# Kernel optimization log

Hardware: AMD Instinct MI355X
Metric: run time of the kernel (lower is better)

Reference implementation:

```python
import jax, jax.numpy as jnp
import numpy as np

B, L, INP, HID, NCLS = 512, 256, 300, 256, 5  # trees, leaves/tree, embed dim, hidden, classes


def setup_inputs() -> dict:
    key = jax.random.key(0)
    ks = jax.random.split(key, 7)
    s_in = 1.0 / np.sqrt(INP).astype(np.float32)
    s_h = 1.0 / np.sqrt(HID).astype(np.float32)
    # W_leaf order: [inp_gate, out_gate, upd_gate]
    # W_nl order:  [inp_ln, inp_rn, fo_l_l, fo_l_r, fo_r_l, fo_r_r, out_ln, out_rn, upd_ln, upd_rn]
    return {
        "embeddings": jax.random.normal(ks[0], (B, L, INP), jnp.float32),
        "W_leaf": jax.random.uniform(ks[1], (3, INP, HID), jnp.float32, -s_in, s_in),
        "b_leaf": jax.random.uniform(ks[2], (3, HID), jnp.float32, -s_in, s_in),
        "W_nl": jax.random.uniform(ks[3], (10, HID, HID), jnp.float32, -s_h, s_h),
        "b_nl": jax.random.uniform(ks[4], (10, HID), jnp.float32, -s_h, s_h),
        "W_out": jax.random.uniform(ks[5], (HID, NCLS), jnp.float32, -s_h, s_h),
        "b_out": jax.random.uniform(ks[6], (NCLS,), jnp.float32, -s_h, s_h),
    }


def reference(embeddings, W_leaf, b_leaf, W_nl, b_nl, W_out, b_out):
    sig, tanh = jax.nn.sigmoid, jnp.tanh
    # ---- leaf nodes (depth 0), batched over all B*L leaves ----
    pre = jnp.einsum('bli,gih->blgh', embeddings, W_leaf) + b_leaf  # [B,L,3,H]
    i_g = sig(pre[:, :, 0])
    o_g = sig(pre[:, :, 1])
    u_g = tanh(pre[:, :, 2])
    c = i_g * u_g                      # [B,L,H]
    h = o_g * sig(c)                   # note: leaf uses sigmoid(cell), as in torch code
    logits = [jnp.einsum('bnh,hc->bnc', h, W_out) + b_out]
    # ---- internal nodes, level-synchronous ----
    Wl = W_nl[0::2]                    # [5,H,H] acting on left hidden
    Wr = W_nl[1::2]                    # [5,H,H] acting on right hidden
    bb = b_nl[0::2] + b_nl[1::2]       # [5,H]
    n = L
    while n > 1:
        lc, rc = c[:, 0::2], c[:, 1::2]
        lh, rh = h[:, 0::2], h[:, 1::2]
        pre = (jnp.einsum('bnh,ghk->bngk', lh, Wl)
               + jnp.einsum('bnh,ghk->bngk', rh, Wr) + bb)  # [B,n/2,5,H]
        inp_g = sig(pre[:, :, 0])
        fol_g = sig(pre[:, :, 1])
        for_g = sig(pre[:, :, 2])
        out_g = sig(pre[:, :, 3])
        upd_g = tanh(pre[:, :, 4])
        c = inp_g * upd_g + fol_g * lc + for_g * rc
        h = out_g * tanh(c)
        logits.append(jnp.einsum('bnh,hc->bnc', h, W_out) + b_out)
        n //= 2
    # per-node class scores for all 2L-1 nodes (leaves first, root last)
    return jnp.concatenate(logits, axis=1)  # [B, 2L-1, NCLS]
```

## Files before the change

### kernel.cpp

```cpp
#include <hip/hip_runtime.h>
#include <hip/hip_bf16.h>


#define HID 256

typedef __attribute__((ext_vector_type(8))) short short8;
typedef __attribute__((ext_vector_type(4))) float f32x4;
typedef __attribute__((ext_vector_type(4))) unsigned short ushort4v;

__device__ __forceinline__ float rcpf(float x) { return __builtin_amdgcn_rcpf(x); }
__device__ __forceinline__ float sigf(float x) { return rcpf(1.0f + __expf(-x)); }
__device__ __forceinline__ float tanhf_(float x) { return 2.0f * rcpf(1.0f + __expf(-2.0f * x)) - 1.0f; }
__device__ __forceinline__ unsigned short f2bf(float f) {
    __hip_bfloat16 b = __float2bfloat16(f);
    return *(unsigned short*)&b;
}
__device__ __forceinline__ void gload_lds16(const void* g, void* l) {
    __builtin_amdgcn_global_load_lds(
        (const __attribute__((address_space(1))) unsigned int*)g,
        (__attribute__((address_space(3))) unsigned int*)l, 16, 0, 0);
}

template <int NG, int K, bool LEAF>
__global__ __launch_bounds__(256, 3) void gemm_gates(
    const unsigned short* __restrict__ A,
    const unsigned short* __restrict__ BT,
    const float* __restrict__ bias,
    const float* __restrict__ cprev,
    float* __restrict__ cout,
    unsigned short* __restrict__ hout,
    const float* __restrict__ W_out,
    float* __restrict__ out,
    int log2n, int off)
{
    constexpr int CS  = 32;
    constexpr int BN  = NG * CS;
    constexpr int NK  = K / 64;
    constexpr int NBW = BN / 32;
    constexpr int ABUF = 128 * 128;

    __shared__ char smem[2 * ABUF + BN * 128];
    char* Bs = smem + 2 * ABUF;

    const int t = threadIdx.x;
    const int lane = t & 63;
    const int w = t >> 6;
    const int wm = w >> 1, wn = w & 1;
    const int row0 = blockIdx.x * 128;
    const int cb = blockIdx.y;

    const int l3 = lane >> 3;
    const unsigned int swsrc = (unsigned int)(((lane & 7) ^ l3) * 16);
    unsigned int a_src[4];
    unsigned int b_src[NBW];
#pragma unroll
    for (int q = 0; q < 4; ++q)
        a_src[q] = (unsigned int)(row0 + (w * 4 + q) * 8 + l3) * (K * 2) + swsrc;
#pragma unroll
    for (int q = 0; q < NBW; ++q)
        b_src[q] = (unsigned int)(cb * BN + (w * NBW + q) * 8 + l3) * (K * 2) + swsrc;

    const int swz0 = ((lane >> 4) ^ (lane & 7)) * 16;
    const int swz1 = (((lane >> 4) + 4) ^ (lane & 7)) * 16;
    const int aoff = (wm * 64 + (lane & 15)) * 128;
    const int boff = (wn * 16 + (lane & 15)) * 128;

    f32x4 acc[4][NG] = {};

    auto STAGE_A = [&](int buf, int kt) {
        char* As = smem + buf * ABUF;
        const unsigned int k0b = (unsigned int)kt * 128;
#pragma unroll
        for (int q = 0; q < 4; ++q)
            gload_lds16((const char*)A + (size_t)(a_src[q] + k0b),
                        As + (w * 4 + q) * 1024);
    };
    auto STAGE_B = [&](int kt) {
        const unsigned int k0b = (unsigned int)kt * 128;
#pragma unroll
        for (int q = 0; q < NBW; ++q)
            gload_lds16((const char*)BT + (size_t)(b_src[q] + k0b),
                        Bs + (w * NBW + q) * 1024);
    };

    STAGE_A(0, 0);
    STAGE_B(0);
    asm volatile("s_waitcnt vmcnt(0)" ::: "memory");
    __builtin_amdgcn_s_barrier();
    asm volatile("" ::: "memory");

#pragma unroll
    for (int kt = 0; kt < NK; ++kt) {
        const int cur = kt & 1;
        if (kt + 1 < NK) STAGE_A(cur ^ 1, kt + 1);
        const char* As = smem + cur * ABUF;
#pragma unroll
        for (int ks = 0; ks < 2; ++ks) {
            const int sw = ks ? swz1 : swz0;
            short8 a[4];
#pragma unroll
            for (int mf = 0; mf < 4; ++mf)
                a[mf] = *(const short8*)(As + aoff + mf * 2048 + sw);
#pragma unroll
            for (int g = 0; g < NG; ++g) {
                short8 b = *(const short8*)(Bs + g * (CS * 128) + boff + sw);
#pragma unroll
                for (int mf = 0; mf < 4; ++mf)
                    acc[mf][g] = __builtin_amdgcn_mfma_f32_16x16x32_bf16(
                        a[mf], b, acc[mf][g], 0, 0, 0);
            }
        }
        asm volatile("" ::: "memory");
        __builtin_amdgcn_s_barrier();
        asm volatile("" ::: "memory");
        if (kt + 1 < NK) {
            STAGE_B(kt + 1);
            asm volatile("s_waitcnt vmcnt(0)" ::: "memory");
        }
        __builtin_amdgcn_s_barrier();
        asm volatile("" ::: "memory");
    }

    float* hs = (float*)smem;
    float* Ws = (float*)(smem + 128 * 33 * 4);
    for (int i = t; i < CS * 5; i += 256) Ws[i] = W_out[cb * CS * 5 + i];

#pragma unroll
    for (int mf = 0; mf < 4; ++mf) {
#pragma unroll
        for (int j = 0; j < 4; ++j) {
            const int rl = wm * 64 + mf * 16 + ((lane >> 4) << 2) + j;
            const int r = row0 + rl;
            const int cl = wn * 16 + (lane & 15);
            const int c = cb * CS + cl;
            float cv, hv;
            if constexpr (LEAF) {
                float p0 = acc[mf][0][j] + bias[c];
                float p1 = acc[mf][1][j] + bias[256 + c];
                float p2 = acc[mf][2][j] + bias[512 + c];
                cv = sigf(p0) * tanhf_(p2);
                hv = sigf(p1) * sigf(cv);
            } else {
                float p0 = acc[mf][0][j] + bias[c];
                float p1 = acc[mf][1][j] + bias[256 + c];
                float p2 = acc[mf][2][j] + bias[512 + c];
                float p3 = acc[mf][3][j] + bias[768 + c];
                float p4 = acc[mf][4][j] + bias[1024 + c];
                float lc = cprev[(size_t)r * 512 + c];
                float rc = cprev[(size_t)r * 512 + 256 + c];
                cv = sigf(p0) * tanhf_(p4) + sigf(p1) * lc + sigf(p2) * rc;
                hv = sigf(p3) * tanhf_(cv);
            }
            cout[(size_t)r * 256 + c] = cv;
            hout[(size_t)r * 256 + c] = f2bf(hv);
            hs[rl * 33 + cl] = hv;
        }
    }
    __syncthreads();

    const int nmask = (1 << log2n) - 1;
    for (int idx = t; idx < 128 * 5; idx += 256) {
        int rl = idx / 5, cls = idx - rl * 5;
        float s = 0.f;
#pragma unroll
        for (int c2 = 0; c2 < CS; ++c2)
            s = fmaf(hs[rl * 33 + c2], Ws[c2 * 5 + cls], s);
        int rg = row0 + rl;
        int b = rg >> log2n, jj = rg & nmask;
        atomicAdd(out + ((size_t)b * 511 + off + jj) * 5 + cls, s);
    }
}

__global__ __launch_bounds__(256) void prep_weights(
    const float* __restrict__ W_leaf, const float* __restrict__ W_nl,
    const float* __restrict__ b_nl, const float* __restrict__ b_out,
    unsigned short* __restrict__ BleafT, unsigned short* __restrict__ BlevT,
    float* __restrict__ bb, float* __restrict__ out)
{
    const int T1 = 768 * 320, T2 = 1280 * 512, T3 = 5 * 256, T4 = 261632 * 5;
    for (int idx = blockIdx.x * 256 + threadIdx.x; idx < T1 + T2 + T3 + T4;
         idx += gridDim.x * 256) {
        if (idx < T1) {
            int colp = idx / 320, k = idx % 320;
            int cbv = colp / 96, rem = colp % 96;
            int g = rem >> 5, cl = rem & 31;
            int c = cbv * 32 + cl;
            float v = (k < 300) ? W_leaf[((size_t)g * 300 + k) * 256 + c] : 0.0f;
            BleafT[(size_t)colp * 320 + k] = f2bf(v);
        } else if (idx < T1 + T2) {
            int i2 = idx - T1;
            int colp = i2 / 512, k = i2 % 512;
            int cb8 = colp / 160, rem = colp % 160;
            int g = rem >> 5, cl = rem & 31;
            int c = cb8 * 32 + cl;
            float v = W_nl[((size_t)(2 * g + (k >= 256)) * 256 + (k & 255)) * 256 + c];
            BlevT[(size_t)colp * 512 + k] = f2bf(v);
        } else if (idx < T1 + T2 + T3) {
            int i3 = idx - T1 - T2;
            bb[i3] = b_nl[(size_t)(i3 >> 8) * 512 + (i3 & 255)] +
                     b_nl[(size_t)(i3 >> 8) * 512 + 256 + (i3 & 255)];
        } else {
            int i4 = idx - T1 - T2 - T3;
            out[i4] = b_out[i4 % 5];
        }
    }
}

__global__ __launch_bounds__(256) void emb_to_bf16(
    const float* __restrict__ emb, unsigned short* __restrict__ embB)
{
    const int total = 131072 * 80;
    for (int idx = blockIdx.x * 256 + threadIdx.x; idx < total;
         idx += gridDim.x * 256) {
        int r = idx / 80, q = idx % 80;
        ushort4v o;
        if (q < 75) {
            const float4 v = *(const float4*)(emb + (size_t)r * 300 + q * 4);
            o.x = f2bf(v.x); o.y = f2bf(v.y); o.z = f2bf(v.z); o.w = f2bf(v.w);
        } else {
            o.x = 0; o.y = 0; o.z = 0; o.w = 0;
        }
        *(ushort4v*)(embB + (size_t)r * 320 + q * 4) = o;
    }
}

extern "C" void kernel_launch(void* const* d_in, const int* in_sizes, int n_in,
                              void* d_out, int out_size, void* d_ws, size_t ws_size,
                              hipStream_t stream) {
    const float* emb    = (const float*)d_in[0];
    const float* W_leaf = (const float*)d_in[1];
    const float* b_leaf = (const float*)d_in[2];
    const float* W_nl   = (const float*)d_in[3];
    const float* b_nl   = (const float*)d_in[4];
    const float* W_out  = (const float*)d_in[5];
    const float* b_out  = (const float*)d_in[6];
    float* out = (float*)d_out;

    char* ws = (char*)d_ws;
    unsigned short* embB   = (unsigned short*)(ws);
    unsigned short* BleafT = (unsigned short*)(ws + 83886080);
    unsigned short* BlevT  = (unsigned short*)(ws + 84377600);
    float*          bb     = (float*)(ws + 85688320);
    float*          cA     = (float*)(ws + 85693440);
    unsigned short* hA     = (unsigned short*)(ws + 219911168);
    float*          cB     = (float*)(ws + 287020032);
    unsigned short* hB     = (unsigned short*)(ws + 354128896);

    prep_weights<<<2048, 256, 0, stream>>>(W_leaf, W_nl, b_nl, b_out,
                                           BleafT, BlevT, bb, out);
    emb_to_bf16<<<2048, 256, 0, stream>>>(emb, embB);

    gemm_gates<3, 320, true><<<dim3(1024, 8), 256, 0, stream>>>(
        embB, BleafT, b_leaf, nullptr, cA, hA, W_out, out, 8, 0);

    const unsigned short* hp = hA;
    const float* cp = cA;
    int off = 256;
    for (int lev = 1; lev <= 8; ++lev) {
        int log2n = 8 - lev;
        int n = 1 << log2n;
        int M = 512 * n;
        float* cd = (lev & 1) ? cB : cA;
        unsigned short* hd = (lev & 1) ? hB : hA;
        gemm_gates<5, 512, false><<<dim3(M / 128, 8), 256, 0, stream>>>(
            hp, BlevT, bb, cp, cd, hd, W_out, out, log2n, off);
        cp = cd;
        hp = hd;
        off += n;
    }
}
```

Before: 512.5 us.

## Add large-tile 512-thread GEMM variant for leaf and early tree levels

Adds a gemm_big kernel using 256x(NG*64) tiles, 8 waves, a unified double-buffered A+B LDS stage and s_setprio around the MFMA bursts. It is used for the leaf level and for internal levels with M>=16384, with a matching column-permuted weight layout. Small levels keep the old 128-row kernel with the original weight layout. The aim is more reuse of each A/B tile and fewer redundant A loads across column blocks. In exchange it uses more LDS and registers per block (acc[8][5]), which cuts occupancy, and it stores two copies of the level weights.

```diff
diff --git a/kernel.cpp b/kernel.cpp
--- a/kernel.cpp
+++ b/kernel.cpp
@@ -22,7 +22,7 @@
 }
 
 template <int NG, int K, bool LEAF>
-__global__ __launch_bounds__(256, 3) void gemm_gates(
+__global__ __launch_bounds__(512, 2) void gemm_big(
     const unsigned short* __restrict__ A,
     const unsigned short* __restrict__ BT,
     const float* __restrict__ bias,
@@ -33,106 +33,96 @@
     float* __restrict__ out,
     int log2n, int off)
 {
-    constexpr int CS  = 32;
-    constexpr int BN  = NG * CS;
-    constexpr int NK  = K / 64;
-    constexpr int NBW = BN / 32;
-    constexpr int ABUF = 128 * 128;
-
-    __shared__ char smem[2 * ABUF + BN * 128];
-    char* Bs = smem + 2 * ABUF;
+    constexpr int BN   = NG * 64;
+    constexpr int NK   = K / 64;
+    constexpr int ABUF = 256 * 128;
+    constexpr int BBUF = BN * 128;
+    constexpr int BUF  = ABUF + BBUF;
+
+    __shared__ char smem[2 * BUF];
 
     const int t = threadIdx.x;
     const int lane = t & 63;
     const int w = t >> 6;
-    const int wm = w >> 1, wn = w & 1;
-    const int row0 = blockIdx.x * 128;
+    const int wm = w >> 2, wn = w & 3;
+    const int row0 = blockIdx.x * 256;
     const int cb = blockIdx.y;
 
     const int l3 = lane >> 3;
     const unsigned int swsrc = (unsigned int)(((lane & 7) ^ l3) * 16);
     unsigned int a_src[4];
-    unsigned int b_src[NBW];
+    unsigned int b_src[NG];
 #pragma unroll
     for (int q = 0; q < 4; ++q)
         a_src[q] = (unsigned int)(row0 + (w * 4 + q) * 8 + l3) * (K * 2) + swsrc;
 #pragma unroll
-    for (int q = 0; q < NBW; ++q)
-        b_src[q] = (unsigned int)(cb * BN + (w * NBW + q) * 8 + l3) * (K * 2) + swsrc;
+    for (int q = 0; q < NG; ++q)
+        b_src[q] = (unsigned int)(cb * BN + (w * NG + q) * 8 + l3) * (K * 2) + swsrc;
 
     const int swz0 = ((lane >> 4) ^ (lane & 7)) * 16;
     const int swz1 = (((lane >> 4) + 4) ^ (lane & 7)) * 16;
-    const int aoff = (wm * 64 + (lane & 15)) * 128;
-    const int boff = (wn * 16 + (lane & 15)) * 128;
-
-    f32x4 acc[4][NG] = {};
-
-    auto STAGE_A = [&](int buf, int kt) {
-        char* As = smem + buf * ABUF;
+    const int aoff = (wm * 128 + (lane & 15)) * 128;
+    const int boff = (wn * (NG * 16) + (lane & 15)) * 128;
+
+    f32x4 acc[8][NG] = {};
+
+    auto STAGE = [&](int buf, int kt) {
+        char* As = smem + buf * BUF;
+        char* Bs = As + ABUF;
         const unsigned int k0b = (unsigned int)kt * 128;
 #pragma unroll
         for (int q = 0; q < 4; ++q)
             gload_lds16((const char*)A + (size_t)(a_src[q] + k0b),
                         As + (w * 4 + q) * 1024);
+#pragma unroll
+        for (int q = 0; q < NG; ++q)
+            gload_lds16((const char*)BT + (size_t)(b_src[q] + k0b),
+                        Bs + (w * NG + q) * 1024);
     };
-    auto STAGE_B = [&](int kt) {
-        const unsigned int k0b = (unsigned int)kt * 128;
-#pragma unroll
-        for (int q = 0; q < NBW; ++q)
-            gload_lds16((const char*)BT + (size_t)(b_src[q] + k0b),
-                        Bs + (w * NBW + q) * 1024);
-    };
-
-    STAGE_A(0, 0);
-    STAGE_B(0);
-    asm volatile("s_waitcnt vmcnt(0)" ::: "memory");
-    __builtin_amdgcn_s_barrier();
-    asm volatile("" ::: "memory");
+
+    STAGE(0, 0);
+    __syncthreads();
 
 #pragma unroll
     for (int kt = 0; kt < NK; ++kt) {
         const int cur = kt & 1;
-        if (kt + 1 < NK) STAGE_A(cur ^ 1, kt + 1);
-        const char* As = smem + cur * ABUF;
+        const char* As = smem + cur * BUF;
+        const char* Bs = As + ABUF;
+        if (kt + 1 < NK) STAGE(cur ^ 1, kt + 1);
 #pragma unroll
         for (int ks = 0; ks < 2; ++ks) {
             const int sw = ks ? swz1 : swz0;
-            short8 a[4];
-#pragma unroll
-            for (int mf = 0; mf < 4; ++mf)
+            short8 a[8], b[NG];
+#pragma unroll
+            for (int mf = 0; mf < 8; ++mf)
                 a[mf] = *(const short8*)(As + aoff + mf * 2048 + sw);
 #pragma unroll
-            for (int g = 0; g < NG; ++g) {
-                short8 b = *(const short8*)(Bs + g * (CS * 128) + boff + sw);
-#pragma unroll
-                for (int mf = 0; mf < 4; ++mf)
+            for (int g = 0; g < NG; ++g)
+                b[g] = *(const short8*)(Bs + boff + g * 2048 + sw);
+            __builtin_amdgcn_s_setprio(1);
+#pragma unroll
+            for (int g = 0; g < NG; ++g)
+#pragma unroll
+                for (int mf = 0; mf < 8; ++mf)
                     acc[mf][g] = __builtin_amdgcn_mfma_f32_16x16x32_bf16(
-                        a[mf], b, acc[mf][g], 0, 0, 0);
-            }
-        }
-        asm volatile("" ::: "memory");
-        __builtin_amdgcn_s_barrier();
-        asm volatile("" ::: "memory");
-        if (kt + 1 < NK) {
-            STAGE_B(kt + 1);
-            asm volatile("s_waitcnt vmcnt(0)" ::: "memory");
-        }
-        __builtin_amdgcn_s_barrier();
-        asm volatile("" ::: "memory");
+                        a[mf], b[g], acc[mf][g], 0, 0, 0);
+            __builtin_amdgcn_s_setprio(0);
+        }
+        __syncthreads();
     }
 
     float* hs = (float*)smem;
-    float* Ws = (float*)(smem + 128 * 33 * 4);
-    for (int i = t; i < CS * 5; i += 256) Ws[i] = W_out[cb * CS * 5 + i];
-
-#pragma unroll
-    for (int mf = 0; mf < 4; ++mf) {
+    float* Ws = (float*)(smem + 256 * 65 * 4);
+    for (int i = t; i < 320; i += 512) Ws[i] = W_out[cb * 320 + i];
+
+    const int cl = wn * 16 + (lane & 15);
+    const int c = cb * 64 + cl;
+#pragma unroll
+    for (int mf = 0; mf < 8; ++mf) {
 #pragma unroll
         for (int j = 0; j < 4; ++j) {
-            const int rl = wm * 64 + mf * 16 + ((lane >> 4) << 2) + j;
+            const int rl = wm * 128 + mf * 16 + ((lane >> 4) << 2) + j;
             const int r = row0 + rl;
-            const int cl = wn * 16 + (lane & 15);
-            const int c = cb * CS + cl;
             float cv, hv;
             if constexpr (LEAF) {
                 float p0 = acc[mf][0][j] + bias[c];
@@ -153,6 +143,147 @@
             }
             cout[(size_t)r * 256 + c] = cv;
             hout[(size_t)r * 256 + c] = f2bf(hv);
+            hs[rl * 65 + cl] = hv;
+        }
+    }
+    __syncthreads();
+
+    const int nmask = (1 << log2n) - 1;
+    for (int idx = t; idx < 256 * 5; idx += 512) {
+        int rl = idx / 5, cls = idx - rl * 5;
+        float s = 0.f;
+#pragma unroll
+        for (int c2 = 0; c2 < 64; ++c2)
+            s = fmaf(hs[rl * 65 + c2], Ws[c2 * 5 + cls], s);
+        int rg = row0 + rl;
+        int b = rg >> log2n, jj = rg & nmask;
+        atomicAdd(out + ((size_t)b * 511 + off + jj) * 5 + cls, s);
+    }
+}
+
+template <int NG, int K>
+__global__ __launch_bounds__(256, 3) void gemm_small(
+    const unsigned short* __restrict__ A,
+    const unsigned short* __restrict__ BT,
+    const float* __restrict__ bias,
+    const float* __restrict__ cprev,
+    float* __restrict__ cout,
+    unsigned short* __restrict__ hout,
+    const float* __restrict__ W_out,
+    float* __restrict__ out,
+    int log2n, int off)
+{
+    constexpr int CS  = 32;
+    constexpr int BN  = NG * CS;
+    constexpr int NK  = K / 64;
+    constexpr int NBW = BN / 32;
+    constexpr int ABUF = 128 * 128;
+
+    __shared__ char smem[2 * ABUF + BN * 128];
+    char* Bs = smem + 2 * ABUF;
+
+    const int t = threadIdx.x;
+    const int lane = t & 63;
+    const int w = t >> 6;
+    const int wm = w >> 1, wn = w & 1;
+    const int row0 = blockIdx.x * 128;
+    const int cb = blockIdx.y;
+
+    const int l3 = lane >> 3;
+    const unsigned int swsrc = (unsigned int)(((lane & 7) ^ l3) * 16);
+    unsigned int a_src[4];
+    unsigned int b_src[NBW];
+#pragma unroll
+    for (int q = 0; q < 4; ++q)
+        a_src[q] = (unsigned int)(row0 + (w * 4 + q) * 8 + l3) * (K * 2) + swsrc;
+#pragma unroll
+    for (int q = 0; q < NBW; ++q)
+        b_src[q] = (unsigned int)(cb * BN + (w * NBW + q) * 8 + l3) * (K * 2) + swsrc;
+
+    const int swz0 = ((lane >> 4) ^ (lane & 7)) * 16;
+    const int swz1 = (((lane >> 4) + 4) ^ (lane & 7)) * 16;
+    const int aoff = (wm * 64 + (lane & 15)) * 128;
+    const int boff = (wn * 16 + (lane & 15)) * 128;
+
+    f32x4 acc[4][NG] = {};
+
+    auto STAGE_A = [&](int buf, int kt) {
+        char* As = smem + buf * ABUF;
+        const unsigned int k0b = (unsigned int)kt * 128;
+#pragma unroll
+        for (int q = 0; q < 4; ++q)
+            gload_lds16((const char*)A + (size_t)(a_src[q] + k0b),
+                        As + (w * 4 + q) * 1024);
+    };
+    auto STAGE_B = [&](int kt) {
+        const unsigned int k0b = (unsigned int)kt * 128;
+#pragma unroll
+        for (int q = 0; q < NBW; ++q)
+            gload_lds16((const char*)BT + (size_t)(b_src[q] + k0b),
+                        Bs + (w * NBW + q) * 1024);
+    };
+
+    STAGE_A(0, 0);
+    STAGE_B(0);
+    asm volatile("s_waitcnt vmcnt(0)" ::: "memory");
+    __builtin_amdgcn_s_barrier();
+    asm volatile("" ::: "memory");
+
+#pragma unroll
+    for (int kt = 0; kt < NK; ++kt) {
+        const int cur = kt & 1;
+        if (kt + 1 < NK) STAGE_A(cur ^ 1, kt + 1);
+        const char* As = smem + cur * ABUF;
+#pragma unroll
+        for (int ks = 0; ks < 2; ++ks) {
+            const int sw = ks ? swz1 : swz0;
+            short8 a[4];
+#pragma unroll
+            for (int mf = 0; mf < 4; ++mf)
+                a[mf] = *(const short8*)(As + aoff + mf * 2048 + sw);
+#pragma unroll
+            for (int g = 0; g < NG; ++g) {
+                short8 b = *(const short8*)(Bs + g * (CS * 128) + boff + sw);
+#pragma unroll
+                for (int mf = 0; mf < 4; ++mf)
+                    acc[mf][g] = __builtin_amdgcn_mfma_f32_16x16x32_bf16(
+                        a[mf], b, acc[mf][g], 0, 0, 0);
+            }
+        }
+        asm volatile("" ::: "memory");
+        __builtin_amdgcn_s_barrier();
+        asm volatile("" ::: "memory");
+        if (kt + 1 < NK) {
+            STAGE_B(kt + 1);
+            asm volatile("s_waitcnt vmcnt(0)" ::: "memory");
+        }
+        __builtin_amdgcn_s_barrier();
+        asm volatile("" ::: "memory");
+    }
+
+    float* hs = (float*)smem;
+    float* Ws = (float*)(smem + 128 * 33 * 4);
+    for (int i = t; i < CS * 5; i += 256) Ws[i] = W_out[cb * CS * 5 + i];
+
+#pragma unroll
+    for (int mf = 0; mf < 4; ++mf) {
+#pragma unroll
+        for (int j = 0; j < 4; ++j) {
+            const int rl = wm * 64 + mf * 16 + ((lane >> 4) << 2) + j;
+            const int r = row0 + rl;
+            const int cl = wn * 16 + (lane & 15);
+            const int c = cb * CS + cl;
+            float p0 = acc[mf][0][j] + bias[c];
+            float p1 = acc[mf][1][j] + bias[256 + c];
+            float p2 = acc[mf][2][j] + bias[512 + c];
+            float p3 = acc[mf][3][j] + bias[768 + c];
+            float p4 = acc[mf][4][j] + bias[1024 + c];
+            float lc = cprev[(size_t)r * 512 + c];
+            float rc = cprev[(size_t)r * 512 + 256 + c];
+            float cv = sigf(p0) * tanhf_(p4) + sigf(p1) * lc + sigf(p2) * rc;
+            float hv = sigf(p3) * tanhf_(cv);
+            cout[(size_t)r * 256 + c] = cv;
+            hout[(size_t)r * 256 + c] = f2bf(hv);
             hs[rl * 33 + cl] = hv;
         }
     }
@@ -174,33 +305,46 @@
 __global__ __launch_bounds__(256) void prep_weights(
     const float* __restrict__ W_leaf, const float* __restrict__ W_nl,
     const float* __restrict__ b_nl, const float* __restrict__ b_out,
-    unsigned short* __restrict__ BleafT, unsigned short* __restrict__ BlevT,
+    unsigned short* __restrict__ BleafT,
+    unsigned short* __restrict__ BlevTn,
+    unsigned short* __restrict__ BlevTo,
     float* __restrict__ bb, float* __restrict__ out)
 {
-    const int T1 = 768 * 320, T2 = 1280 * 512, T3 = 5 * 256, T4 = 261632 * 5;
-    for (int idx = blockIdx.x * 256 + threadIdx.x; idx < T1 + T2 + T3 + T4;
+    const int T1 = 768 * 320, T2 = 1280 * 512, T3 = 1280 * 512;
+    const int T4 = 5 * 256, T5 = 261632 * 5;
+    for (int idx = blockIdx.x * 256 + threadIdx.x; idx < T1 + T2 + T3 + T4 + T5;
          idx += gridDim.x * 256) {
         if (idx < T1) {
             int colp = idx / 320, k = idx % 320;
-            int cbv = colp / 96, rem = colp % 96;
-            int g = rem >> 5, cl = rem & 31;
-            int c = cbv * 32 + cl;
+            int cbv = colp / 192, r = colp % 192;
+            int wn = r / 48, r2 = r % 48;
+            int g = r2 >> 4, cl = r2 & 15;
+            int c = cbv * 64 + wn * 16 + cl;
             float v = (k < 300) ? W_leaf[((size_t)g * 300 + k) * 256 + c] : 0.0f;
             BleafT[(size_t)colp * 320 + k] = f2bf(v);
         } else if (idx < T1 + T2) {
             int i2 = idx - T1;
             int colp = i2 / 512, k = i2 % 512;
-            int cb8 = colp / 160, rem = colp % 160;
-            int g = rem >> 5, cl = rem & 31;
+            int cbv = colp / 320, r = colp % 320;
+            int wn = r / 80, r2 = r % 80;
+            int g = r2 >> 4, cl = r2 & 15;
+            int c = cbv * 64 + wn * 16 + cl;
+            float v = W_nl[((size_t)(2 * g + (k >= 256)) * 256 + (k & 255)) * 256 + c];
+            BlevTn[(size_t)colp * 512 + k] = f2bf(v);
+        } else if (idx < T1 + T2 + T3) {
+            int i2 = idx - T1 - T2;
+            int colp = i2 / 512, k = i2 % 512;
+            int cb8 = colp / 160, r = colp % 160;
+            int g = r >> 5, cl = r & 31;
             int c = cb8 * 32 + cl;
             float v = W_nl[((size_t)(2 * g + (k >= 256)) * 256 + (k & 255)) * 256 + c];
-            BlevT[(size_t)colp * 512 + k] = f2bf(v);
-        } else if (idx < T1 + T2 + T3) {
-            int i3 = idx - T1 - T2;
+            BlevTo[(size_t)colp * 512 + k] = f2bf(v);
+        } else if (idx < T1 + T2 + T3 + T4) {
+            int i3 = idx - T1 - T2 - T3;
             bb[i3] = b_nl[(size_t)(i3 >> 8) * 512 + (i3 & 255)] +
                      b_nl[(size_t)(i3 >> 8) * 512 + 256 + (i3 & 255)];
         } else {
-            int i4 = idx - T1 - T2 - T3;
+            int i4 = idx - T1 - T2 - T3 - T4;
             out[i4] = b_out[i4 % 5];
         }
     }
@@ -239,18 +383,19 @@
     char* ws = (char*)d_ws;
     unsigned short* embB   = (unsigned short*)(ws);
     unsigned short* BleafT = (unsigned short*)(ws + 83886080);
-    unsigned short* BlevT  = (unsigned short*)(ws + 84377600);
-    float*          bb     = (float*)(ws + 85688320);
-    float*          cA     = (float*)(ws + 85693440);
-    unsigned short* hA     = (unsigned short*)(ws + 219911168);
-    float*          cB     = (float*)(ws + 287020032);
-    unsigned short* hB     = (unsigned short*)(ws + 354128896);
+    unsigned short* BlevTn = (unsigned short*)(ws + 84377600);
+    unsigned short* BlevTo = (unsigned short*)(ws + 85688320);
+    float*          bb     = (float*)(ws + 86999040);
+    float*          cA     = (float*)(ws + 87004160);
+    unsigned short* hA     = (unsigned short*)(ws + 221221888);
+    float*          cB     = (float*)(ws + 288330752);
+    unsigned short* hB     = (unsigned short*)(ws + 355439616);
 
     prep_weights<<<2048, 256, 0, stream>>>(W_leaf, W_nl, b_nl, b_out,
-                                           BleafT, BlevT, bb, out);
+                                           BleafT, BlevTn, BlevTo, bb, out);
     emb_to_bf16<<<2048, 256, 0, stream>>>(emb, embB);
 
-    gemm_gates<3, 320, true><<<dim3(1024, 8), 256, 0, stream>>>(
+    gemm_big<3, 320, true><<<dim3(512, 4), 512, 0, stream>>>(
         embB, BleafT, b_leaf, nullptr, cA, hA, W_out, out, 8, 0);
 
     const unsigned short* hp = hA;
@@ -262,8 +407,13 @@
         int M = 512 * n;
         float* cd = (lev & 1) ? cB : cA;
         unsigned short* hd = (lev & 1) ? hB : hA;
-        gemm_gates<5, 512, false><<<dim3(M / 128, 8), 256, 0, stream>>>(
-            hp, BlevT, bb, cp, cd, hd, W_out, out, log2n, off);
+        if (M >= 16384) {
+            gemm_big<5, 512, false><<<dim3(M / 256, 4), 512, 0, stream>>>(
+                hp, BlevTn, bb, cp, cd, hd, W_out, out, log2n, off);
+        } else {
+            gemm_small<5, 512><<<dim3(M / 128, 8), 256, 0, stream>>>(
+                hp, BlevTo, bb, cp, cd, hd, W_out, out, log2n, off);
+        }
         cp = cd;
         hp = hd;
         off += n;
```

Measured after the change: 506.0 us. About the same (-1.3%).
